# Optimization experiments

Hardware: AMD Instinct MI355X
Metric: run time of the kernel (lower is better)

The kernel has to match this reference:

```python
import jax, jax.numpy as jnp
import numpy as np

B, V, H = 16384, 1024, 256


def setup_inputs() -> dict:
    key = jax.random.key(0)
    k1, k2 = jax.random.split(key)
    # binary spin configurations in {0,1}
    batch = jax.random.bernoulli(k1, 0.5, (B, V)).astype(jnp.float32)
    # small weights + negative hidden bias keep exp(log p*) finite in fp32
    weights_amp = jax.random.normal(k2, (H, V), dtype=jnp.float32) * (0.05 / np.sqrt(V))
    visible_bias_amp = jnp.zeros((V,), dtype=jnp.float32)
    hidden_bias_amp = -5.0 * jnp.ones((H,), dtype=jnp.float32)
    return {
        'batch': batch,
        'weights_amp': weights_amp,
        'visible_bias_amp': visible_bias_amp,
        'hidden_bias_amp': hidden_bias_amp,
        'k': 8,
    }


def _gibbs_sampling_amp(v0, W, vb, hb, k, key):
    """k steps of block Gibbs sampling, vectorized over the whole batch [B,V]."""
    keys = jax.random.split(key, 2 * k).reshape(k, 2)

    def step(v, ks):
        ph = jax.nn.sigmoid(v @ W.T + hb)                      # [B,H]
        h = (jax.random.uniform(ks[0], ph.shape) < ph).astype(v.dtype)
        pv = jax.nn.sigmoid(h @ W + vb)                        # [B,V]
        v = (jax.random.uniform(ks[1], pv.shape) < pv).astype(v.dtype)
        return v, None

    vk, _ = jax.lax.scan(step, v0, keys)
    return vk


def reference(batch, weights_amp, visible_bias_amp, hidden_bias_amp, k):
    W, vb, hb = weights_amp, visible_bias_amp, hidden_bias_amp
    nbatch = batch.shape[0]
    key = jax.random.key(42)

    vk = _gibbs_sampling_amp(batch, W, vb, hb, k, key)          # [B,V]

    ph0 = jax.nn.sigmoid(batch @ W.T + hb)                      # [B,H] positive-phase hidden probs
    pre_k = vk @ W.T + hb                                       # [B,H]
    phk = jax.nn.sigmoid(pre_k)                                 # [B,H] negative-phase hidden probs

    # unnormalized_probability_amp(vk) = exp(vk.vb + sum_j softplus((W vk + hb)_j))
    log_p = vk @ vb + jax.nn.softplus(pre_k).sum(axis=-1)       # [B]
    inv_norm = jnp.exp(-log_p) / nbatch                         # 1 / (len(batch) * p*(vk))

    # g_W = sum_b [outer(phk_b, vk_b) - outer(ph0_b, v0_b)] / norm_b
    g_w = (jnp.einsum('b,bh,bv->hv', inv_norm, phk, vk)
           - jnp.einsum('b,bh,bv->hv', inv_norm, ph0, batch))   # [H,V]
    g_vb = jnp.einsum('b,bv->v', inv_norm, vk - batch)          # [V]
    g_hb = jnp.einsum('b,bh->h', inv_norm, phk - ph0)           # [H]

    return jnp.concatenate([g_w.ravel(), g_vb, g_hb])
```

## Files before the change

kernel.cpp:

```cpp
#include <hip/hip_runtime.h>
#include <stdint.h>

#define B_DIM 16384
#define V_DIM 1024
#define H_DIM 256
#define K_STEPS 8

typedef short bf16x8 __attribute__((ext_vector_type(8)));
typedef float f32x4 __attribute__((ext_vector_type(4)));

__host__ __device__ inline uint32_t rotl32(uint32_t v, int r) {
    return (v << r) | (v >> (32 - r));
}

__host__ __device__ inline void threefry2x32(uint32_t k0, uint32_t k1,
                                             uint32_t x0, uint32_t x1,
                                             uint32_t* o0, uint32_t* o1) {
    uint32_t k2 = k0 ^ k1 ^ 0x1BD11BDAu;
    x0 += k0; x1 += k1;
#define TF_RND(r) { x0 += x1; x1 = rotl32(x1, (r)); x1 ^= x0; }
    TF_RND(13) TF_RND(15) TF_RND(26) TF_RND(6)
    x0 += k1; x1 += k2 + 1u;
    TF_RND(17) TF_RND(29) TF_RND(16) TF_RND(24)
    x0 += k2; x1 += k0 + 2u;
    TF_RND(13) TF_RND(15) TF_RND(26) TF_RND(6)
    x0 += k0; x1 += k1 + 3u;
    TF_RND(17) TF_RND(29) TF_RND(16) TF_RND(24)
    x0 += k1; x1 += k2 + 4u;
    TF_RND(13) TF_RND(15) TF_RND(26) TF_RND(6)
    x0 += k2; x1 += k0 + 5u;
#undef TF_RND
    *o0 = x0; *o1 = x1;
}

__device__ inline float tf_uniform(uint32_t key0, uint32_t key1, uint32_t e) {
    uint32_t o0, o1;
    threefry2x32(key0, key1, 0u, e, &o0, &o1);
    uint32_t bits = o0 ^ o1;
    return __uint_as_float((bits >> 9) | 0x3f800000u) - 1.0f;
}

__device__ inline uint16_t bf16_rn(float f) {
    uint32_t u = __float_as_uint(f);
    uint32_t r = u + 0x7FFFu + ((u >> 16) & 1u);
    return (uint16_t)(r >> 16);
}
__device__ inline float bf16_to_f32(uint16_t h) {
    return __uint_as_float(((uint32_t)h) << 16);
}

__device__ inline void gload_lds16(const void* g, void* l) {
    __builtin_amdgcn_global_load_lds((const __attribute__((address_space(1))) uint32_t*)g,
                                     (__attribute__((address_space(3))) uint32_t*)l, 16, 0, 0);
}

template <int MODE>
__global__ __launch_bounds__(256, 4) void mfma_gemm(
    const ushort* __restrict__ A, const ushort* __restrict__ Bhi,
    const ushort* __restrict__ Blo, const float* __restrict__ bias,
    void* __restrict__ out, ushort* __restrict__ out2,
    int N, int K, int k_slice, uint32_t key0, uint32_t key1) {
    __shared__ __align__(16) ushort As[64 * 32];
    __shared__ __align__(16) ushort Bs[64 * 32];
    __shared__ __align__(16) ushort Bs2[64 * 32];

    const int tid = threadIdx.x;
    const int lane = tid & 63;
    const int w = tid >> 6;
    const int m0 = blockIdx.x * 64;
    const int n0 = blockIdx.y * 64;
    const int kbase = blockIdx.z * k_slice;

    f32x4 acc[2][2] = {};

    const int wm = (w & 1) * 32;
    const int wn = (w >> 1) * 32;
    const int q = lane >> 4;
    const int l15 = lane & 15;
    const int srow = lane >> 2;
    const int scol = (lane & 3) * 8;

    const size_t arow = (size_t)(m0 + w * 16 + srow) * K;
    const size_t brow = (size_t)(n0 + w * 16 + srow) * K;

    for (int kt = 0; kt < k_slice; kt += 32) {
        const int k0 = kbase + kt;
        gload_lds16(&A[arow + k0 + scol], &As[w * 512]);
        gload_lds16(&Bhi[brow + k0 + scol], &Bs[w * 512]);
        if (MODE != 2) gload_lds16(&Blo[brow + k0 + scol], &Bs2[w * 512]);
        __syncthreads();
        bf16x8 af[2], bh[2], bl[2];
#pragma unroll
        for (int i = 0; i < 2; ++i)
            af[i] = *(const bf16x8*)&As[(wm + i * 16 + l15) * 32 + q * 8];
#pragma unroll
        for (int j = 0; j < 2; ++j) {
            bh[j] = *(const bf16x8*)&Bs[(wn + j * 16 + l15) * 32 + q * 8];
            if (MODE != 2) bl[j] = *(const bf16x8*)&Bs2[(wn + j * 16 + l15) * 32 + q * 8];
        }
#pragma unroll
        for (int i = 0; i < 2; ++i)
#pragma unroll
            for (int j = 0; j < 2; ++j) {
                acc[i][j] = __builtin_amdgcn_mfma_f32_16x16x32_bf16(af[i], bh[j], acc[i][j], 0, 0, 0);
                if (MODE != 2)
                    acc[i][j] = __builtin_amdgcn_mfma_f32_16x16x32_bf16(af[i], bl[j], acc[i][j], 0, 0, 0);
            }
        __syncthreads();
    }

    const int orow = q * 4;
#pragma unroll
    for (int i = 0; i < 2; ++i) {
#pragma unroll
        for (int j = 0; j < 2; ++j) {
            int col = n0 + wn + j * 16 + l15;
            float bv = (MODE == 2) ? 0.0f : bias[col];
#pragma unroll
            for (int r = 0; r < 4; ++r) {
                int row = m0 + wm + i * 16 + orow + r;
                float val = acc[i][j][r] + bv;
                if (MODE == 0 || MODE == 3) {
                    float sg = 1.0f / (1.0f + expf(-val));
                    uint32_t e = (uint32_t)row * (uint32_t)N + (uint32_t)col;
                    float u = tf_uniform(key0, key1, e);
                    ((ushort*)out)[(size_t)row * N + col] = (u < sg) ? (ushort)0x3F80 : (ushort)0;
                    if (MODE == 3) out2[(size_t)row * N + col] = bf16_rn(sg);
                } else if (MODE == 1) {
                    float sg = 1.0f / (1.0f + expf(-val));
                    ((ushort*)out)[(size_t)row * N + col] = bf16_rn(sg);
                } else {
                    atomicAdd(&((float*)out)[(size_t)row * N + col], val);
                }
            }
        }
    }
}

__global__ void wsplit_kernel(const float* __restrict__ W, ushort* __restrict__ whi,
                              ushort* __restrict__ wlo, ushort* __restrict__ wthi,
                              ushort* __restrict__ wtlo) {
    int idx = blockIdx.x * 256 + threadIdx.x;
    int h = idx >> 10, v = idx & 1023;
    float w = W[idx];
    ushort hi = bf16_rn(w);
    float fhi = bf16_to_f32(hi);
    ushort lo = bf16_rn(w - fhi);
    whi[idx] = hi; wlo[idx] = lo;
    wthi[v * H_DIM + h] = hi; wtlo[v * H_DIM + h] = lo;
}

__global__ void tobf16_kernel(const float* __restrict__ src, ushort* __restrict__ dst) {
    int idx = blockIdx.x * 256 + threadIdx.x;
    float4 f = ((const float4*)src)[idx];
    ushort4 o;
    o.x = bf16_rn(f.x); o.y = bf16_rn(f.y); o.z = bf16_rn(f.z); o.w = bf16_rn(f.w);
    ((ushort4*)dst)[idx] = o;
}

__global__ __launch_bounds__(256) void lognorm_kernel(
    const ushort* __restrict__ phk, const ushort* __restrict__ vk,
    const float* __restrict__ vb, float* __restrict__ inv) {
    int b = blockIdx.x;
    int tid = threadIdx.x;
    float p = bf16_to_f32(phk[(size_t)b * H_DIM + tid]);
    float s = -log1pf(-p);
    for (int j = tid; j < V_DIM; j += 256)
        s += bf16_to_f32(vk[(size_t)b * V_DIM + j]) * vb[j];
    for (int off = 32; off > 0; off >>= 1) s += __shfl_down(s, off, 64);
    __shared__ float wsum[4];
    int lane = tid & 63, wid = tid >> 6;
    if (lane == 0) wsum[wid] = s;
    __syncthreads();
    if (tid == 0) {
        float t = wsum[0] + wsum[1] + wsum[2] + wsum[3];
        inv[b] = expf(-t) * (1.0f / 16384.0f);
    }
}

__global__ void build_At(const ushort* __restrict__ P, const float* __restrict__ inv,
                         float sgn, ushort* __restrict__ At) {
    __shared__ float T[64][65];
    int c = threadIdx.x & 63;
    int rb = threadIdx.x >> 6;
    int b0 = blockIdx.x * 64;
    int h0 = blockIdx.y * 64;
    for (int r = rb; r < 64; r += 4) {
        int b = b0 + r;
        T[c][r] = sgn * inv[b] * bf16_to_f32(P[(size_t)b * H_DIM + h0 + c]);
    }
    __syncthreads();
    for (int r = rb; r < 64; r += 4)
        At[(size_t)(h0 + r) * B_DIM + b0 + c] = bf16_rn(T[r][c]);
}

__global__ void build_Bt(const ushort* __restrict__ Sb, const float* __restrict__ Sf,
                         int use_f32, ushort* __restrict__ Bt) {
    __shared__ ushort T[64][65];
    int c = threadIdx.x & 63;
    int rb = threadIdx.x >> 6;
    int b0 = blockIdx.x * 64;
    int v0 = blockIdx.y * 64;
    for (int r = rb; r < 64; r += 4) {
        int b = b0 + r;
        T[c][r] = use_f32 ? bf16_rn(Sf[(size_t)b * V_DIM + v0 + c])
                          : Sb[(size_t)b * V_DIM + v0 + c];
    }
    __syncthreads();
    for (int r = rb; r < 64; r += 4)
        Bt[(size_t)(v0 + r) * B_DIM + b0 + c] = T[r][c];
}

__global__ void gvb_kernel(const ushort* __restrict__ vk, const ushort* __restrict__ vbat,
                           const float* __restrict__ inv, float* __restrict__ gvb) {
    int col = blockIdx.x * 256 + threadIdx.x;
    int b0 = blockIdx.y * 512;
    float acc = 0.0f;
    for (int r = 0; r < 512; ++r) {
        int b = b0 + r;
        acc += inv[b] * (bf16_to_f32(vk[(size_t)b * V_DIM + col]) -
                         bf16_to_f32(vbat[(size_t)b * V_DIM + col]));
    }
    atomicAdd(&gvb[col], acc);
}

__global__ void ghb_kernel(const ushort* __restrict__ phk, const ushort* __restrict__ ph0,
                           const float* __restrict__ inv, float* __restrict__ ghb) {
    int col = threadIdx.x;
    int b0 = blockIdx.x * 256;
    float acc = 0.0f;
    for (int r = 0; r < 256; ++r) {
        int b = b0 + r;
        acc += inv[b] * (bf16_to_f32(phk[(size_t)b * H_DIM + col]) -
                         bf16_to_f32(ph0[(size_t)b * H_DIM + col]));
    }
    atomicAdd(&ghb[col], acc);
}

extern "C" void kernel_launch(void* const* d_in, const int* in_sizes, int n_in,
                              void* d_out, int out_size, void* d_ws, size_t ws_size,
                              hipStream_t stream) {
    const float* batch = (const float*)d_in[0];
    const float* W = (const float*)d_in[1];
    const float* vb = (const float*)d_in[2];
    const float* hb = (const float*)d_in[3];

    char* base = (char*)d_ws;
    ushort* w_hi  = (ushort*)(base + 0);
    ushort* w_lo  = (ushort*)(base + 524288);
    ushort* wt_hi = (ushort*)(base + 1048576);
    ushort* wt_lo = (ushort*)(base + 1572864);
    ushort* v_cur = (ushort*)(base + 2097152);
    float*  inv   = (float*)(base + 35651584);
    ushort* h_cur = (ushort*)(base + 35717120);
    ushort* At    = h_cur;
    ushort* batch_bf = (ushort*)(base + 44105728);
    ushort* Bt    = batch_bf;
    ushort* ph0b  = (ushort*)(base + 77660160);
    ushort* phkb  = (ushort*)(base + 86048768);

    float* gw  = (float*)d_out;
    float* gvb = gw + (size_t)H_DIM * V_DIM;
    float* ghb = gvb + V_DIM;

    hipMemsetAsync(d_out, 0, (size_t)out_size * sizeof(float), stream);

    uint32_t sk0[16], sk1[16];
    for (int n = 0; n < 16; ++n) threefry2x32(0u, 42u, 0u, (uint32_t)n, &sk0[n], &sk1[n]);

    wsplit_kernel<<<dim3(1024), dim3(256), 0, stream>>>(W, w_hi, w_lo, wt_hi, wt_lo);
    tobf16_kernel<<<dim3(B_DIM * V_DIM / 4 / 256), dim3(256), 0, stream>>>(batch, batch_bf);

    for (int i = 0; i < K_STEPS; ++i) {
        const ushort* vin = (i == 0) ? batch_bf : v_cur;
        if (i == 0) {
            mfma_gemm<3><<<dim3(B_DIM / 64, H_DIM / 64, 1), dim3(256), 0, stream>>>(
                vin, w_hi, w_lo, hb, h_cur, ph0b, H_DIM, V_DIM, V_DIM, sk0[0], sk1[0]);
        } else {
            mfma_gemm<0><<<dim3(B_DIM / 64, H_DIM / 64, 1), dim3(256), 0, stream>>>(
                vin, w_hi, w_lo, hb, h_cur, nullptr, H_DIM, V_DIM, V_DIM, sk0[2 * i], sk1[2 * i]);
        }
        mfma_gemm<0><<<dim3(B_DIM / 64, V_DIM / 64, 1), dim3(256), 0, stream>>>(
            h_cur, wt_hi, wt_lo, vb, v_cur, nullptr, V_DIM, H_DIM, H_DIM, sk0[2 * i + 1], sk1[2 * i + 1]);
    }
    mfma_gemm<1><<<dim3(B_DIM / 64, H_DIM / 64, 1), dim3(256), 0, stream>>>(
        v_cur, w_hi, w_lo, hb, phkb, nullptr, H_DIM, V_DIM, V_DIM, 0u, 0u);

    lognorm_kernel<<<dim3(B_DIM), dim3(256), 0, stream>>>(phkb, v_cur, vb, inv);
    ghb_kernel<<<dim3(B_DIM / 256), dim3(256), 0, stream>>>(phkb, ph0b, inv, ghb);
    gvb_kernel<<<dim3(V_DIM / 256, B_DIM / 512), dim3(256), 0, stream>>>(v_cur, batch_bf, inv, gvb);

    build_At<<<dim3(B_DIM / 64, H_DIM / 64), dim3(256), 0, stream>>>(phkb, inv, 1.0f, At);
    build_Bt<<<dim3(B_DIM / 64, V_DIM / 64), dim3(256), 0, stream>>>(v_cur, nullptr, 0, Bt);
    mfma_gemm<2><<<dim3(H_DIM / 64, V_DIM / 64, 16), dim3(256), 0, stream>>>(
        At, Bt, nullptr, nullptr, gw, nullptr, V_DIM, B_DIM, 1024, 0u, 0u);
    build_At<<<dim3(B_DIM / 64, H_DIM / 64), dim3(256), 0, stream>>>(ph0b, inv, -1.0f, At);
    build_Bt<<<dim3(B_DIM / 64, V_DIM / 64), dim3(256), 0, stream>>>(nullptr, batch, 1, Bt);
    mfma_gemm<2><<<dim3(H_DIM / 64, V_DIM / 64, 16), dim3(256), 0, stream>>>(
        At, Bt, nullptr, nullptr, gw, nullptr, V_DIM, B_DIM, 1024, 0u, 0u);
}
```

Before: 1.030 ms.

## Load MFMA operands directly from global memory in Gibbs GEMMs, dropping LDS staging

```diff
diff --git a/kernel.cpp b/kernel.cpp
--- a/kernel.cpp
+++ b/kernel.cpp
@@ -54,15 +54,80 @@
                                      (__attribute__((address_space(3))) uint32_t*)l, 16, 0, 0);
 }
 
-template <int MODE>
-__global__ __launch_bounds__(256, 4) void mfma_gemm(
+template <int MODE, int KTOT, int NN>
+__global__ __launch_bounds__(256, 6) void mfma_gemm_direct(
     const ushort* __restrict__ A, const ushort* __restrict__ Bhi,
     const ushort* __restrict__ Blo, const float* __restrict__ bias,
-    void* __restrict__ out, ushort* __restrict__ out2,
-    int N, int K, int k_slice, uint32_t key0, uint32_t key1) {
+    ushort* __restrict__ out, ushort* __restrict__ out2,
+    uint32_t key0, uint32_t key1) {
+    const int tid = threadIdx.x;
+    const int lane = tid & 63;
+    const int w = tid >> 6;
+    const int m0 = blockIdx.x * 64;
+    const int n0 = blockIdx.y * 64;
+
+    const int wm = (w & 1) * 32;
+    const int wn = (w >> 1) * 32;
+    const int q = lane >> 4;
+    const int l15 = lane & 15;
+
+    const ushort* a0p = A + (size_t)(m0 + wm + l15) * KTOT + q * 8;
+    const ushort* a1p = a0p + 16 * KTOT;
+    const ushort* bh0p = Bhi + (size_t)(n0 + wn + l15) * KTOT + q * 8;
+    const ushort* bh1p = bh0p + 16 * KTOT;
+    const ushort* bl0p = Blo + (size_t)(n0 + wn + l15) * KTOT + q * 8;
+    const ushort* bl1p = bl0p + 16 * KTOT;
+
+    f32x4 acc[2][2] = {};
+
+#pragma unroll 8
+    for (int kt = 0; kt < KTOT; kt += 32) {
+        bf16x8 af[2], bh[2], bl[2];
+        af[0] = *(const bf16x8*)(a0p + kt);
+        af[1] = *(const bf16x8*)(a1p + kt);
+        bh[0] = *(const bf16x8*)(bh0p + kt);
+        bh[1] = *(const bf16x8*)(bh1p + kt);
+        bl[0] = *(const bf16x8*)(bl0p + kt);
+        bl[1] = *(const bf16x8*)(bl1p + kt);
+#pragma unroll
+        for (int i = 0; i < 2; ++i)
+#pragma unroll
+            for (int j = 0; j < 2; ++j) {
+                acc[i][j] = __builtin_amdgcn_mfma_f32_16x16x32_bf16(af[i], bh[j], acc[i][j], 0, 0, 0);
+                acc[i][j] = __builtin_amdgcn_mfma_f32_16x16x32_bf16(af[i], bl[j], acc[i][j], 0, 0, 0);
+            }
+    }
+
+    const int orow = q * 4;
+#pragma unroll
+    for (int i = 0; i < 2; ++i) {
+#pragma unroll
+        for (int j = 0; j < 2; ++j) {
+            int col = n0 + wn + j * 16 + l15;
+            float bv = bias[col];
+#pragma unroll
+            for (int r = 0; r < 4; ++r) {
+                int row = m0 + wm + i * 16 + orow + r;
+                float val = acc[i][j][r] + bv;
+                float sg = 1.0f / (1.0f + expf(-val));
+                if (MODE == 0 || MODE == 3) {
+                    uint32_t e = (uint32_t)row * (uint32_t)NN + (uint32_t)col;
+                    float u = tf_uniform(key0, key1, e);
+                    out[(size_t)row * NN + col] = (u < sg) ? (ushort)0x3F80 : (ushort)0;
+                    if (MODE == 3) out2[(size_t)row * NN + col] = bf16_rn(sg);
+                } else {
+                    out[(size_t)row * NN + col] = bf16_rn(sg);
+                }
+            }
+        }
+    }
+}
+
+__global__ __launch_bounds__(256, 4) void mfma_gemm_acc(
+    const ushort* __restrict__ A, const ushort* __restrict__ Bt,
+    float* __restrict__ out, int N, int K, int k_slice) {
     __shared__ __align__(16) ushort As[64 * 32];
     __shared__ __align__(16) ushort Bs[64 * 32];
-    __shared__ __align__(16) ushort Bs2[64 * 32];
 
     const int tid = threadIdx.x;
     const int lane = tid & 63;
@@ -86,55 +151,34 @@
     for (int kt = 0; kt < k_slice; kt += 32) {
         const int k0 = kbase + kt;
         gload_lds16(&A[arow + k0 + scol], &As[w * 512]);
-        gload_lds16(&Bhi[brow + k0 + scol], &Bs[w * 512]);
-        if (MODE != 2) gload_lds16(&Blo[brow + k0 + scol], &Bs2[w * 512]);
+        gload_lds16(&Bt[brow + k0 + scol], &Bs[w * 512]);
         __syncthreads();
-        bf16x8 af[2], bh[2], bl[2];
+        bf16x8 af[2], bf[2];
+#pragma unroll
+        for (int i = 0; i < 2; ++i) {
+            af[i] = *(const bf16x8*)&As[(wm + i * 16 + l15) * 32 + q * 8];
+            bf[i] = *(const bf16x8*)&Bs[(wn + i * 16 + l15) * 32 + q * 8];
+        }
 #pragma unroll
         for (int i = 0; i < 2; ++i)
-            af[i] = *(const bf16x8*)&As[(wm + i * 16 + l15) * 32 + q * 8];
-#pragma unroll
-        for (int j = 0; j < 2; ++j) {
-            bh[j] = *(const bf16x8*)&Bs[(wn + j * 16 + l15) * 32 + q * 8];
-            if (MODE != 2) bl[j] = *(const bf16x8*)&Bs2[(wn + j * 16 + l15) * 32 + q * 8];
-        }
-#pragma unroll
-        for (int i = 0; i < 2; ++i)
-#pragma unroll
-            for (int j = 0; j < 2; ++j) {
-                acc[i][j] = __builtin_amdgcn_mfma_f32_16x16x32_bf16(af[i], bh[j], acc[i][j], 0, 0, 0);
-                if (MODE != 2)
-                    acc[i][j] = __builtin_amdgcn_mfma_f32_16x16x32_bf16(af[i], bl[j], acc[i][j], 0, 0, 0);
-            }
+#pragma unroll
+            for (int j = 0; j < 2; ++j)
+                acc[i][j] = __builtin_amdgcn_mfma_f32_16x16x32_bf16(af[i], bf[j], acc[i][j], 0, 0, 0);
         __syncthreads();
     }
 
     const int orow = q * 4;
 #pragma unroll
-    for (int i = 0; i < 2; ++i) {
+    for (int i = 0; i < 2; ++i)
 #pragma unroll
         for (int j = 0; j < 2; ++j) {
             int col = n0 + wn + j * 16 + l15;
-            float bv = (MODE == 2) ? 0.0f : bias[col];
 #pragma unroll
             for (int r = 0; r < 4; ++r) {
                 int row = m0 + wm + i * 16 + orow + r;
-                float val = acc[i][j][r] + bv;
-                if (MODE == 0 || MODE == 3) {
-                    float sg = 1.0f / (1.0f + expf(-val));
-                    uint32_t e = (uint32_t)row * (uint32_t)N + (uint32_t)col;
-                    float u = tf_uniform(key0, key1, e);
-                    ((ushort*)out)[(size_t)row * N + col] = (u < sg) ? (ushort)0x3F80 : (ushort)0;
-                    if (MODE == 3) out2[(size_t)row * N + col] = bf16_rn(sg);
-                } else if (MODE == 1) {
-                    float sg = 1.0f / (1.0f + expf(-val));
-                    ((ushort*)out)[(size_t)row * N + col] = bf16_rn(sg);
-                } else {
-                    atomicAdd(&((float*)out)[(size_t)row * N + col], val);
-                }
+                atomicAdd(&out[(size_t)row * N + col], acc[i][j][r]);
             }
         }
-    }
 }
 
 __global__ void wsplit_kernel(const float* __restrict__ W, ushort* __restrict__ whi,
@@ -274,17 +318,17 @@
     for (int i = 0; i < K_STEPS; ++i) {
         const ushort* vin = (i == 0) ? batch_bf : v_cur;
         if (i == 0) {
-            mfma_gemm<3><<<dim3(B_DIM / 64, H_DIM / 64, 1), dim3(256), 0, stream>>>(
-                vin, w_hi, w_lo, hb, h_cur, ph0b, H_DIM, V_DIM, V_DIM, sk0[0], sk1[0]);
+            mfma_gemm_direct<3, V_DIM, H_DIM><<<dim3(B_DIM / 64, H_DIM / 64), dim3(256), 0, stream>>>(
+                vin, w_hi, w_lo, hb, h_cur, ph0b, sk0[0], sk1[0]);
         } else {
-            mfma_gemm<0><<<dim3(B_DIM / 64, H_DIM / 64, 1), dim3(256), 0, stream>>>(
-                vin, w_hi, w_lo, hb, h_cur, nullptr, H_DIM, V_DIM, V_DIM, sk0[2 * i], sk1[2 * i]);
+            mfma_gemm_direct<0, V_DIM, H_DIM><<<dim3(B_DIM / 64, H_DIM / 64), dim3(256), 0, stream>>>(
+                vin, w_hi, w_lo, hb, h_cur, nullptr, sk0[2 * i], sk1[2 * i]);
         }
-        mfma_gemm<0><<<dim3(B_DIM / 64, V_DIM / 64, 1), dim3(256), 0, stream>>>(
-            h_cur, wt_hi, wt_lo, vb, v_cur, nullptr, V_DIM, H_DIM, H_DIM, sk0[2 * i + 1], sk1[2 * i + 1]);
-    }
-    mfma_gemm<1><<<dim3(B_DIM / 64, H_DIM / 64, 1), dim3(256), 0, stream>>>(
-        v_cur, w_hi, w_lo, hb, phkb, nullptr, H_DIM, V_DIM, V_DIM, 0u, 0u);
+        mfma_gemm_direct<0, H_DIM, V_DIM><<<dim3(B_DIM / 64, V_DIM / 64), dim3(256), 0, stream>>>(
+            h_cur, wt_hi, wt_lo, vb, v_cur, nullptr, sk0[2 * i + 1], sk1[2 * i + 1]);
+    }
+    mfma_gemm_direct<1, V_DIM, H_DIM><<<dim3(B_DIM / 64, H_DIM / 64), dim3(256), 0, stream>>>(
+        v_cur, w_hi, w_lo, hb, phkb, nullptr, 0u, 0u);
 
     lognorm_kernel<<<dim3(B_DIM), dim3(256), 0, stream>>>(phkb, v_cur, vb, inv);
     ghb_kernel<<<dim3(B_DIM / 256), dim3(256), 0, stream>>>(phkb, ph0b, inv, ghb);
@@ -292,10 +336,10 @@
 
     build_At<<<dim3(B_DIM / 64, H_DIM / 64), dim3(256), 0, stream>>>(phkb, inv, 1.0f, At);
     build_Bt<<<dim3(B_DIM / 64, V_DIM / 64), dim3(256), 0, stream>>>(v_cur, nullptr, 0, Bt);
-    mfma_gemm<2><<<dim3(H_DIM / 64, V_DIM / 64, 16), dim3(256), 0, stream>>>(
-        At, Bt, nullptr, nullptr, gw, nullptr, V_DIM, B_DIM, 1024, 0u, 0u);
+    mfma_gemm_acc<<<dim3(H_DIM / 64, V_DIM / 64, 16), dim3(256), 0, stream>>>(
+        At, Bt, gw, V_DIM, B_DIM, 1024);
     build_At<<<dim3(B_DIM / 64, H_DIM / 64), dim3(256), 0, stream>>>(ph0b, inv, -1.0f, At);
     build_Bt<<<dim3(B_DIM / 64, V_DIM / 64), dim3(256), 0, stream>>>(nullptr, batch, 1, Bt);
-    mfma_gemm<2><<<dim3(H_DIM / 64, V_DIM / 64, 16), dim3(256), 0, stream>>>(
-        At, Bt, nullptr, nullptr, gw, nullptr, V_DIM, B_DIM, 1024, 0u, 0u);
-}
+    mfma_gemm_acc<<<dim3(H_DIM / 64, V_DIM / 64, 16), dim3(256), 0, stream>>>(
+        At, Bt, gw, V_DIM, B_DIM, 1024);
+}
```

Result: slower. 1.838 ms (+78.4%).
